# Optimization experiments

Hardware: AMD Instinct MI355X
Metric: run time of the kernel (lower is better)

Reference implementation:

```python
import jax, jax.numpy as jnp
import numpy as np

DIM = 1024
HEADS = 16
DIM_HEAD = 64
INNER = HEADS * DIM_HEAD
SCALE = DIM_HEAD ** -0.5


def rotate_half(t):
    # '... (j d) -> ... j d' with j=2: split last dim in half
    x1, x2 = jnp.split(t, 2, axis=-1)
    return jnp.concatenate((-x2, x1), axis=-1)


def rotary_pos(n, d, dtype):
    inv_freq = 1.0 / (10000.0 ** (jnp.arange(0, d, 2, dtype=jnp.float32) / d))
    freqs = jnp.arange(n, dtype=jnp.float32)[:, None] * inv_freq[None, :]  # (n, d/2)
    return jnp.concatenate((freqs, freqs), axis=-1).astype(dtype)  # (n, d)


def apply_rope(pos, t):
    return t * jnp.cos(pos) + rotate_half(t) * jnp.sin(pos)


def setup_inputs() -> dict:
    key = jax.random.key(0)
    ks = jax.random.split(key, 5)
    x = jax.random.normal(ks[0], (2, 2048, DIM), dtype=jnp.float32)
    gamma = jnp.ones((DIM,), dtype=jnp.float32)
    beta = jnp.zeros((DIM,), dtype=jnp.float32)
    Wq = jax.random.normal(ks[1], (DIM, INNER), dtype=jnp.float32) * 0.02
    Wkv = jax.random.normal(ks[2], (DIM, 2 * INNER), dtype=jnp.float32) * 0.02
    Wo = jax.random.normal(ks[3], (INNER, DIM), dtype=jnp.float32) * 0.02
    return {"x": x, "gamma": gamma, "beta": beta, "Wq": Wq, "Wkv": Wkv, "Wo": Wo}


def reference(x, gamma, beta, Wq, Wkv, Wo):
    b, n, _ = x.shape
    # LayerNorm with learned gamma, fixed-zero beta buffer
    mu = jnp.mean(x, axis=-1, keepdims=True)
    var = jnp.var(x, axis=-1, keepdims=True)
    xn = (x - mu) / jnp.sqrt(var + 1e-5) * gamma + beta

    q = xn @ Wq                       # (b, n, inner)
    kv = xn @ Wkv
    k, v = jnp.split(kv, 2, axis=-1)

    def to_heads(t):
        return t.reshape(b, n, HEADS, DIM_HEAD).transpose(0, 2, 1, 3)  # b h n d

    q, k, v = map(to_heads, (q, k, v))

    pos = rotary_pos(n, DIM_HEAD, x.dtype)  # (n, d)
    q = apply_rope(pos, q)
    k = apply_rope(pos, k)

    q = q * SCALE
    sim = jnp.einsum('bhid,bhjd->bhij', q, k)

    neg = -jnp.finfo(sim.dtype).max
    causal_mask = jnp.triu(jnp.ones((n, n), dtype=bool), k=1)
    sim = jnp.where(causal_mask, neg, sim)

    attn = jax.nn.softmax(sim, axis=-1)
    out = jnp.einsum('bhij,bhjd->bhid', attn, v)
    out = out.transpose(0, 2, 1, 3).reshape(b, n, INNER)
    return out @ Wo
```

## Files before the change

### kernel.cpp

```cpp
#include <hip/hip_runtime.h>
#include <stdint.h>

typedef unsigned short u16;
typedef __attribute__((ext_vector_type(8))) short short8;
typedef __attribute__((ext_vector_type(4))) float floatx4;
typedef __attribute__((ext_vector_type(4))) unsigned short u16x4;
typedef __attribute__((ext_vector_type(2))) unsigned int uint2v;

__device__ __forceinline__ float bf2f(u16 v) {
  union { uint32_t u; float f; } x; x.u = ((uint32_t)v) << 16; return x.f;
}
__device__ __forceinline__ u16 f2bf(float f) {
  union { float f; uint32_t u; } x; x.f = f;
  uint32_t r = x.u + 0x7fffu + ((x.u >> 16) & 1u);
  return (u16)(r >> 16);
}
__device__ __forceinline__ uint32_t fu(float f) {
  union { float f; uint32_t u; } x; x.f = f; return x.u;
}

#define GL2LDS(g, l)                                                          \
  __builtin_amdgcn_global_load_lds(                                           \
      (const __attribute__((address_space(1))) void*)(g),                     \
      (__attribute__((address_space(3))) void*)(l), 16, 0, 0)

#define WAITBAR(N)                                                            \
  asm volatile("s_waitcnt vmcnt(" #N ")\n\ts_barrier" ::: "memory")
#define BARX asm volatile("s_barrier" ::: "memory")
#define VM0BARX asm volatile("s_waitcnt vmcnt(0)\n\ts_barrier" ::: "memory")

__global__ __launch_bounds__(256) void prep_k(const float* __restrict__ x,
                                              const float* __restrict__ gamma,
                                              const float* __restrict__ beta,
                                              const float* __restrict__ Wq,
                                              const float* __restrict__ Wkv,
                                              const float* __restrict__ Wo,
                                              u16* __restrict__ xn,
                                              u16* __restrict__ wqkvT,
                                              u16* __restrict__ woT) {
  int bid = blockIdx.x;
  int t = threadIdx.x;
  if (bid < 4096) {
    int row = bid;
    const float* xr = x + (size_t)row * 1024;
    float4 xv = *(const float4*)(xr + t * 4);
    float v0 = xv.x, v1 = xv.y, v2 = xv.z, v3 = xv.w;
    float s = v0 + v1 + v2 + v3;
    float s2 = v0 * v0 + v1 * v1 + v2 * v2 + v3 * v3;
#pragma unroll
    for (int d = 1; d < 64; d <<= 1) {
      s += __shfl_xor(s, d, 64);
      s2 += __shfl_xor(s2, d, 64);
    }
    __shared__ float red[8];
    int lane = t & 63, wv = t >> 6;
    if (lane == 0) { red[wv] = s; red[4 + wv] = s2; }
    __syncthreads();
    s = red[0] + red[1] + red[2] + red[3];
    s2 = red[4] + red[5] + red[6] + red[7];
    float mu = s * (1.0f / 1024.0f);
    float var = s2 * (1.0f / 1024.0f) - mu * mu;
    float rstd = rsqrtf(var + 1e-5f);
    float4 gv = *(const float4*)(gamma + t * 4);
    float4 bv = *(const float4*)(beta + t * 4);
    u16x4 ov;
    ov.x = f2bf((v0 - mu) * rstd * gv.x + bv.x);
    ov.y = f2bf((v1 - mu) * rstd * gv.y + bv.y);
    ov.z = f2bf((v2 - mu) * rstd * gv.z + bv.z);
    ov.w = f2bf((v3 - mu) * rstd * gv.w + bv.w);
    *(u16x4*)(xn + (size_t)row * 1024 + t * 4) = ov;
  } else {
    __shared__ float tile[32][33];
    int wb = bid - 4096;
    const float* in;
    u16* outp;
    int C;
    if (wb < 1024) { in = Wq; outp = wqkvT; C = 1024; }
    else if (wb < 3072) { wb -= 1024; in = Wkv; outp = wqkvT + 1024 * 1024; C = 2048; }
    else { wb -= 3072; in = Wo; outp = woT; C = 1024; }
    int nbx = C >> 5;
    int c0 = (wb % nbx) * 32, r0 = (wb / nbx) * 32;
    int tx = t & 31, ty = t >> 5;
#pragma unroll
    for (int i = 0; i < 32; i += 8)
      tile[ty + i][tx] = in[(size_t)(r0 + ty + i) * C + c0 + tx];
    __syncthreads();
#pragma unroll
    for (int i = 0; i < 32; i += 8)
      outp[(size_t)(c0 + ty + i) * 1024 + r0 + tx] = f2bf(tile[tx][ty + i]);
  }
}

__global__ __launch_bounds__(512, 1) void gemm_qkv_k(const u16* __restrict__ A,
                                                     const u16* __restrict__ BT,
                                                     u16* __restrict__ C) {
  __shared__ __align__(16) u16 sA[2][128 * 64];
  __shared__ __align__(16) u16 sB[2][384 * 64];
  int tid = threadIdx.x;
  int w = tid >> 6, l = tid & 63;
  int lr = l & 15, lq = l >> 4;
  int wm = w >> 1, wn = w & 1;
  int bm = blockIdx.y * 128;
  int bn = blockIdx.x * 384;
  floatx4 acc[2][12] = {};
  int gcol = ((tid & 7) ^ ((tid >> 3) & 7)) * 8;
  int strow = tid >> 3;
  int t8 = tid * 8;
  const u16* gA = A + (size_t)(bm + strow) * 1024 + gcol;
  const u16* gB = BT + (size_t)(bn + strow) * 1024 + gcol;
  int csw = (lr & 7) << 3;
  int ar = (wm * 32 + lr) * 64;
  int br = (wn * 192 + lr) * 64;

#define ST_A(bi)                                                              \
  { GL2LDS(gA, &sA[bi][t8]); GL2LDS(gA + 65536, &sA[bi][t8 + 4096]); }
#define ST_B(bi)                                                              \
  { GL2LDS(gB, &sB[bi][t8]);                                                  \
    GL2LDS(gB + 65536, &sB[bi][t8 + 4096]);                                   \
    GL2LDS(gB + 131072, &sB[bi][t8 + 8192]);                                  \
    GL2LDS(gB + 196608, &sB[bi][t8 + 12288]);                                 \
    GL2LDS(gB + 262144, &sB[bi][t8 + 16384]);                                 \
    GL2LDS(gB + 327680, &sB[bi][t8 + 20480]); }
#define HALF(p, kh)                                                           \
  {                                                                           \
    int co_ = ((kh)*32 + lq * 8) ^ csw;                                       \
    short8 a0_ = *(const short8*)&sA[p][ar + co_];                            \
    short8 a1_ = *(const short8*)&sA[p][ar + 1024 + co_];                     \
    _Pragma("unroll") for (int g = 0; g < 3; g++) {                           \
      short8 b0_ = *(const short8*)&sB[p][br + (g * 4 + 0) * 1024 + co_];     \
      short8 b1_ = *(const short8*)&sB[p][br + (g * 4 + 1) * 1024 + co_];     \
      short8 b2_ = *(const short8*)&sB[p][br + (g * 4 + 2) * 1024 + co_];     \
      short8 b3_ = *(const short8*)&sB[p][br + (g * 4 + 3) * 1024 + co_];     \
      acc[0][g*4+0] = __builtin_amdgcn_mfma_f32_16x16x32_bf16(a0_, b0_, acc[0][g*4+0], 0, 0, 0); \
      acc[1][g*4+0] = __builtin_amdgcn_mfma_f32_16x16x32_bf16(a1_, b0_, acc[1][g*4+0], 0, 0, 0); \
      acc[0][g*4+1] = __builtin_amdgcn_mfma_f32_16x16x32_bf16(a0_, b1_, acc[0][g*4+1], 0, 0, 0); \
      acc[1][g*4+1] = __builtin_amdgcn_mfma_f32_16x16x32_bf16(a1_, b1_, acc[1][g*4+1], 0, 0, 0); \
      acc[0][g*4+2] = __builtin_amdgcn_mfma_f32_16x16x32_bf16(a0_, b2_, acc[0][g*4+2], 0, 0, 0); \
      acc[1][g*4+2] = __builtin_amdgcn_mfma_f32_16x16x32_bf16(a1_, b2_, acc[1][g*4+2], 0, 0, 0); \
      acc[0][g*4+3] = __builtin_amdgcn_mfma_f32_16x16x32_bf16(a0_, b3_, acc[0][g*4+3], 0, 0, 0); \
      acc[1][g*4+3] = __builtin_amdgcn_mfma_f32_16x16x32_bf16(a1_, b3_, acc[1][g*4+3], 0, 0, 0); \
    }                                                                         \
  }
#define KT(p, q, DOST)                                                        \
  {                                                                           \
    if (DOST) { ST_A(q); ST_B(q); gA += 64; gB += 64; }                       \
    BARX; __builtin_amdgcn_s_setprio(1);                                      \
    HALF(p, 0);                                                               \
    __builtin_amdgcn_s_setprio(0); BARX;                                      \
    __builtin_amdgcn_s_setprio(1);                                            \
    HALF(p, 1);                                                               \
    __builtin_amdgcn_s_setprio(0); VM0BARX;                                   \
  }

  ST_A(0); ST_B(0); gA += 64; gB += 64;
  VM0BARX;
#pragma unroll 1
  for (int t = 0; t < 7; ++t) {
    KT(0, 1, 1);
    KT(1, 0, 1);
  }
  KT(0, 1, 1);
  KT(1, 0, 0);

#pragma unroll
  for (int nig = 0; nig < 3; nig++) {
    int col0 = bn + wn * 192 + nig * 64;
    int sec = col0 >> 10;
    if (sec == 2) {
#pragma unroll
      for (int p4 = 0; p4 < 4; p4++) {
        int ni = nig * 4 + p4;
        int col = col0 + p4 * 16 + lr;
        int cv = col - 2048;
#pragma unroll
        for (int mi = 0; mi < 2; mi++) {
          int row = bm + wm * 32 + mi * 16 + lq * 4;
          int bq = row >> 11;
          int n = row & 2047;
          int bh = (bq << 4) | (cv >> 6);
          int d = cv & 63;
          size_t L = ((size_t)(bh * 64 + d) << 11) + n;
          u16x4 ov;
          ov.x = f2bf(acc[mi][ni][0]);
          ov.y = f2bf(acc[mi][ni][1]);
          ov.z = f2bf(acc[mi][ni][2]);
          ov.w = f2bf(acc[mi][ni][3]);
          *(u16x4*)(C + (L >> 10) * 3072 + 2048 + (L & 1023)) = ov;
        }
      }
    } else {
      float QS = (sec == 0) ? 0.125f * 1.44269504088896f : 1.0f;
#pragma unroll
      for (int np = 0; np < 2; np++) {
        int i = np * 16 + lr;
        float invf = exp2f(-(float)i * 0.4152410118609203f);
#pragma unroll
        for (int mi = 0; mi < 2; mi++)
#pragma unroll
          for (int r = 0; r < 4; r++) {
            int row = bm + wm * 32 + mi * 16 + lq * 4 + r;
            int n = row & 2047;
            float ang = (float)n * invf;
            float s_, c_;
            __sincosf(ang, &s_, &c_);
            float x1 = acc[mi][nig * 4 + np][r];
            float x2 = acc[mi][nig * 4 + np + 2][r];
            int col = col0 + np * 16 + lr;
            C[(size_t)row * 3072 + col] = f2bf((x1 * c_ - x2 * s_) * QS);
            C[(size_t)row * 3072 + col + 32] = f2bf((x2 * c_ + x1 * s_) * QS);
          }
      }
    }
  }
}

__global__ __launch_bounds__(256) void gemm64_bf16_k(const u16* __restrict__ A,
                                                     const u16* __restrict__ BT,
                                                     float* __restrict__ C,
                                                     int K, int lda, int ldc) {
  __shared__ __align__(16) u16 lA[3][64 * 32];
  __shared__ __align__(16) u16 lB[3][128 * 32];
  int tid = threadIdx.x;
  int bm = blockIdx.y * 64;
  int bn = blockIdx.x * 128;
  int w = tid >> 6, l = tid & 63;
  int wm = (w >> 1) * 32, wn = (w & 1) * 64;
  int lr = l & 15, lq = l >> 4;
  floatx4 acc[2][4] = {};
  int sr = w * 16 + (l >> 2);
  int sc = (l & 3) * 8;
  int sds = sr * 32 + sc;
  const u16* pA0 = A + (size_t)(bm + sr) * lda + sc;
  const u16* pB0 = BT + (size_t)(bn + sr) * K + sc;
  const u16* pB1 = pB0 + (size_t)64 * K;
  int ao[2], bo[4];
#pragma unroll
  for (int i = 0; i < 2; i++) ao[i] = (wm + i * 16 + lr) * 32 + lq * 8;
#pragma unroll
  for (int i = 0; i < 4; i++) bo[i] = (wn + i * 16 + lr) * 32 + lq * 8;

#define STAGE_O(bi)                                                           \
  {                                                                           \
    GL2LDS(pA0, &lA[bi][sds]);                                                \
    GL2LDS(pB0, &lB[bi][sds]);                                                \
    GL2LDS(pB1, &lB[bi][sds + 2048]);                                         \
    pA0 += 32; pB0 += 32; pB1 += 32;                                          \
  }
#define COMPUTE_O(bi)                                                         \
  {                                                                           \
    short8 afr[2], bfr[4];                                                    \
    _Pragma("unroll") for (int i = 0; i < 2; i++)                             \
        afr[i] = *(const short8*)(&lA[bi][ao[i]]);                            \
    _Pragma("unroll") for (int i = 0; i < 4; i++)                             \
        bfr[i] = *(const short8*)(&lB[bi][bo[i]]);                            \
    _Pragma("unroll") for (int mi = 0; mi < 2; mi++)                          \
        _Pragma("unroll") for (int ni = 0; ni < 4; ni++)                      \
            acc[mi][ni] = __builtin_amdgcn_mfma_f32_16x16x32_bf16(            \
                afr[mi], bfr[ni], acc[mi][ni], 0, 0, 0);                      \
  }

  STAGE_O(0);
  STAGE_O(1);
#pragma unroll 1
  for (int t = 0; t < 10; ++t) {
    WAITBAR(3); STAGE_O(2); COMPUTE_O(0);
    WAITBAR(3); STAGE_O(0); COMPUTE_O(1);
    WAITBAR(3); STAGE_O(1); COMPUTE_O(2);
  }
  WAITBAR(3); COMPUTE_O(0);
  WAITBAR(0); COMPUTE_O(1);

#pragma unroll
  for (int mi = 0; mi < 2; mi++)
#pragma unroll
    for (int ni = 0; ni < 4; ni++)
#pragma unroll
      for (int r = 0; r < 4; r++) {
        int row = bm + wm + mi * 16 + lq * 4 + r;
        int col = bn + wn + ni * 16 + lr;
        C[(size_t)row * ldc + col] = acc[mi][ni][r];
      }
}

#define LPT 64
#define FIXM 4.0f
__device__ __forceinline__ void attn_tile2(const u16* lK, const u16* lV, u16* lp,
                                           const short8* aq, floatx4* o,
                                           float& l_i, int lr, int lq,
                                           bool diag, int q0, int k0g,
                                           short8 ones) {
  floatx4 s[4];
#pragma unroll
  for (int ni = 0; ni < 4; ni++) {
    floatx4 a = {};
#pragma unroll
    for (int kc = 0; kc < 2; kc++) {
      int R = ni * 16 + lr;
      int c8 = (kc * 4 + lq) ^ (R & 7);
      short8 kf = *(const short8*)&lK[R * 64 + c8 * 8];
      a = __builtin_amdgcn_mfma_f32_16x16x32_bf16(kf, aq[kc], a, 0, 0, 0);
    }
    s[ni] = a;
  }
  if (diag) {
    int qg = q0 + lr;
#pragma unroll
    for (int ni = 0; ni < 4; ni++)
#pragma unroll
      for (int r = 0; r < 4; r++) {
        int kg = k0g + ni * 16 + lq * 4 + r;
        if (kg > qg) s[ni][r] = -1e30f;
      }
  }
  int swz = (lr & 7) << 3;
#pragma unroll
  for (int ni = 0; ni < 4; ni++) {
    float p0 = exp2f(s[ni][0] - FIXM), p1 = exp2f(s[ni][1] - FIXM);
    float p2 = exp2f(s[ni][2] - FIXM), p3 = exp2f(s[ni][3] - FIXM);
    uint2v dw;
    dw.x = __builtin_amdgcn_perm(fu(p1), fu(p0), 0x07060302u);
    dw.y = __builtin_amdgcn_perm(fu(p3), fu(p2), 0x07060302u);
    *(uint2v*)&lp[lr * LPT + ((ni * 16 + lq * 4) ^ swz)] = dw;
  }
  short8 pb0 = *(const short8*)&lp[lr * LPT + ((lq * 8) ^ swz)];
  short8 pb1 = *(const short8*)&lp[lr * LPT + ((32 + lq * 8) ^ swz)];
  floatx4 z = {};
  z = __builtin_amdgcn_mfma_f32_16x16x32_bf16(ones, pb0, z, 0, 0, 0);
  z = __builtin_amdgcn_mfma_f32_16x16x32_bf16(ones, pb1, z, 0, 0, 0);
  l_i += z[0];
#pragma unroll
  for (int di = 0; di < 4; di++) {
    int R = di * 16 + lr;
    int c80 = lq ^ (R & 7);
    int c81 = (4 + lq) ^ (R & 7);
    short8 v0 = *(const short8*)&lV[R * 64 + c80 * 8];
    o[di] = __builtin_amdgcn_mfma_f32_16x16x32_bf16(v0, pb0, o[di], 0, 0, 0);
    short8 v1 = *(const short8*)&lV[R * 64 + c81 * 8];
    o[di] = __builtin_amdgcn_mfma_f32_16x16x32_bf16(v1, pb1, o[di], 0, 0, 0);
  }
}

__global__ __launch_bounds__(256) void attn_k(const u16* __restrict__ qkv,
                                              u16* __restrict__ out) {
  __shared__ __align__(16) u16 lK[2][64 * 64];
  __shared__ __align__(16) u16 lV[2][64 * 64];
  __shared__ __align__(16) u16 lP[4][16 * LPT];
  int bh = blockIdx.x;
  int b = bh >> 4, h = bh & 15;
  int y = blockIdx.y;
  int g = y >> 3, o_ = y & 7;
  int j = (g & 1) ? ((g << 3) + 7 - o_) : y;
  int tid = threadIdx.x;
  int w = tid >> 6, l = tid & 63;
  int lr = l & 15, lq = l >> 4;
  int q0 = j * 64 + w * 16;
  const u16* qb = qkv + (size_t)b * 2048 * 3072 + h * 64;
  const u16* kb = qkv + (size_t)b * 2048 * 3072 + 1024 + h * 64;
  int bh64 = bh * 64;
  short8 aq[2];
  aq[0] = *(const short8*)(qb + (size_t)(q0 + lr) * 3072 + lq * 8);
  aq[1] = *(const short8*)(qb + (size_t)(q0 + lr) * 3072 + 32 + lq * 8);
  short8 ones;
#pragma unroll
  for (int i = 0; i < 8; i++) ones[i] = (short)0x3F80;
  floatx4 o[4] = {};
  float l_ = 0.0f;
  int srow8 = l >> 3;
  int sc8 = (l & 7) ^ srow8;
  u16* lp = &lP[w][0];
  auto stage = [&](int bufi, int kt) {
#pragma unroll
    for (int c = 0; c < 2; c++) {
      int m = w + c * 4;
      int row = m * 8 + srow8;
      GL2LDS(kb + (size_t)(kt * 64 + row) * 3072 + sc8 * 8, &lK[bufi][m * 512]);
      int nn = kt * 64 + sc8 * 8;
      GL2LDS(qkv + (size_t)((bh64 + row) * 2 + (nn >> 10)) * 3072 + 2048 +
                 (nn & 1023),
             &lV[bufi][m * 512]);
    }
  };
  stage(0, 0);
  for (int kt = 0; kt <= j; ++kt) {
    int cur = kt & 1;
    __syncthreads();
    if (kt < j) stage(cur ^ 1, kt + 1);
    attn_tile2(lK[cur], lV[cur], lp, aq, o, l_, lr, lq, kt == j, q0, kt * 64,
               ones);
  }
  float rl = 1.0f / l_;
#pragma unroll
  for (int di = 0; di < 4; di++) {
    uint2v dw;
    u16 a0 = f2bf(o[di][0] * rl), a1 = f2bf(o[di][1] * rl);
    u16 a2 = f2bf(o[di][2] * rl), a3 = f2bf(o[di][3] * rl);
    dw.x = (uint32_t)a0 | ((uint32_t)a1 << 16);
    dw.y = (uint32_t)a2 | ((uint32_t)a3 << 16);
    int dcol = h * 64 + di * 16 + lq * 4;
    *(uint2v*)(out + ((size_t)(b * 2048 + q0 + lr)) * 1024 + dcol) = dw;
  }
}

extern "C" void kernel_launch(void* const* d_in, const int* in_sizes, int n_in,
                              void* d_out, int out_size, void* d_ws, size_t ws_size,
                              hipStream_t stream) {
  const float* x = (const float*)d_in[0];
  const float* gamma = (const float*)d_in[1];
  const float* beta = (const float*)d_in[2];
  const float* Wq = (const float*)d_in[3];
  const float* Wkv = (const float*)d_in[4];
  const float* Wo = (const float*)d_in[5];
  float* out = (float*)d_out;
  char* ws = (char*)d_ws;

  u16* qkv = (u16*)(ws);
  u16* wqkvT = (u16*)(ws + 25165824);
  u16* woT = (u16*)(ws + 31457280);
  u16* xn = (u16*)(ws + 33554432);
  u16* attn_out = xn;

  prep_k<<<8192, 256, 0, stream>>>(x, gamma, beta, Wq, Wkv, Wo, xn, wqkvT, woT);
  gemm_qkv_k<<<dim3(8, 32), 512, 0, stream>>>(xn, wqkvT, qkv);
  attn_k<<<dim3(32, 32), 256, 0, stream>>>(qkv, attn_out);
  gemm64_bf16_k<<<dim3(8, 64), 256, 0, stream>>>(attn_out, woT, out, 1024, 1024, 1024);
}
```

Measured before the change: 186.6 us.

## Pair causal query tiles per block to balance attention work

```diff
diff --git a/kernel.cpp b/kernel.cpp
--- a/kernel.cpp
+++ b/kernel.cpp
@@ -347,24 +347,25 @@
   __shared__ __align__(16) u16 lP[4][16 * LPT];
   int bh = blockIdx.x;
   int b = bh >> 4, h = bh & 15;
-  int y = blockIdx.y;
-  int g = y >> 3, o_ = y & 7;
-  int j = (g & 1) ? ((g << 3) + 7 - o_) : y;
+  int p = blockIdx.y;
   int tid = threadIdx.x;
   int w = tid >> 6, l = tid & 63;
   int lr = l & 15, lq = l >> 4;
-  int q0 = j * 64 + w * 16;
+  int q0A = p * 64 + w * 16;
+  int q0B = (31 - p) * 64 + w * 16;
   const u16* qb = qkv + (size_t)b * 2048 * 3072 + h * 64;
   const u16* kb = qkv + (size_t)b * 2048 * 3072 + 1024 + h * 64;
   int bh64 = bh * 64;
-  short8 aq[2];
-  aq[0] = *(const short8*)(qb + (size_t)(q0 + lr) * 3072 + lq * 8);
-  aq[1] = *(const short8*)(qb + (size_t)(q0 + lr) * 3072 + 32 + lq * 8);
+  short8 aqA[2], aqB[2];
+  aqA[0] = *(const short8*)(qb + (size_t)(q0A + lr) * 3072 + lq * 8);
+  aqA[1] = *(const short8*)(qb + (size_t)(q0A + lr) * 3072 + 32 + lq * 8);
+  aqB[0] = *(const short8*)(qb + (size_t)(q0B + lr) * 3072 + lq * 8);
+  aqB[1] = *(const short8*)(qb + (size_t)(q0B + lr) * 3072 + 32 + lq * 8);
   short8 ones;
 #pragma unroll
   for (int i = 0; i < 8; i++) ones[i] = (short)0x3F80;
-  floatx4 o[4] = {};
-  float l_ = 0.0f;
+  floatx4 oA[4] = {}, oB[4] = {};
+  float lA_ = 0.0f, lB_ = 0.0f;
   int srow8 = l >> 3;
   int sc8 = (l & 7) ^ srow8;
   u16* lp = &lP[w][0];
@@ -381,23 +382,37 @@
     }
   };
   stage(0, 0);
-  for (int kt = 0; kt <= j; ++kt) {
-    int cur = kt & 1;
+  int cur = 0;
+#pragma unroll 1
+  for (int s = 0; s < 33; ++s) {
     __syncthreads();
-    if (kt < j) stage(cur ^ 1, kt + 1);
-    attn_tile2(lK[cur], lV[cur], lp, aq, o, l_, lr, lq, kt == j, q0, kt * 64,
-               ones);
-  }
-  float rl = 1.0f / l_;
+    if (s < 32) {
+      int nk = (s < p) ? (s + 1) : (s - p);
+      stage(cur ^ 1, nk);
+    }
+    if (s <= p)
+      attn_tile2(lK[cur], lV[cur], lp, aqA, oA, lA_, lr, lq, s == p, q0A,
+                 s * 64, ones);
+    else
+      attn_tile2(lK[cur], lV[cur], lp, aqB, oB, lB_, lr, lq, s == 32, q0B,
+                 (s - p - 1) * 64, ones);
+    cur ^= 1;
+  }
+  float rlA = 1.0f / lA_, rlB = 1.0f / lB_;
 #pragma unroll
   for (int di = 0; di < 4; di++) {
-    uint2v dw;
-    u16 a0 = f2bf(o[di][0] * rl), a1 = f2bf(o[di][1] * rl);
-    u16 a2 = f2bf(o[di][2] * rl), a3 = f2bf(o[di][3] * rl);
-    dw.x = (uint32_t)a0 | ((uint32_t)a1 << 16);
-    dw.y = (uint32_t)a2 | ((uint32_t)a3 << 16);
+    uint2v dwA, dwB;
+    u16 a0 = f2bf(oA[di][0] * rlA), a1 = f2bf(oA[di][1] * rlA);
+    u16 a2 = f2bf(oA[di][2] * rlA), a3 = f2bf(oA[di][3] * rlA);
+    dwA.x = (uint32_t)a0 | ((uint32_t)a1 << 16);
+    dwA.y = (uint32_t)a2 | ((uint32_t)a3 << 16);
+    u16 b0 = f2bf(oB[di][0] * rlB), b1 = f2bf(oB[di][1] * rlB);
+    u16 b2 = f2bf(oB[di][2] * rlB), b3 = f2bf(oB[di][3] * rlB);
+    dwB.x = (uint32_t)b0 | ((uint32_t)b1 << 16);
+    dwB.y = (uint32_t)b2 | ((uint32_t)b3 << 16);
     int dcol = h * 64 + di * 16 + lq * 4;
-    *(uint2v*)(out + ((size_t)(b * 2048 + q0 + lr)) * 1024 + dcol) = dw;
+    *(uint2v*)(out + ((size_t)(b * 2048 + q0A + lr)) * 1024 + dcol) = dwA;
+    *(uint2v*)(out + ((size_t)(b * 2048 + q0B + lr)) * 1024 + dcol) = dwB;
   }
 }
 
@@ -421,6 +436,6 @@
 
   prep_k<<<8192, 256, 0, stream>>>(x, gamma, beta, Wq, Wkv, Wo, xn, wqkvT, woT);
   gemm_qkv_k<<<dim3(8, 32), 512, 0, stream>>>(xn, wqkvT, qkv);
-  attn_k<<<dim3(32, 32), 256, 0, stream>>>(qkv, attn_out);
+  attn_k<<<dim3(32, 16), 256, 0, stream>>>(qkv, attn_out);
   gemm64_bf16_k<<<dim3(8, 64), 256, 0, stream>>>(attn_out, woT, out, 1024, 1024, 1024);
 }
```

Measured after the change: 190.9 us. +2.3%, slower.
